# Kernel tuning notes

Measured on AMD Instinct MI355X. Metric: run time of the kernel, lower is better.

The kernel has to match this reference:

```python
import jax, jax.numpy as jnp
import numpy as np


def cheb_mats(N: int, degree: int):
    """Analysis/synthesis Chebyshev matrices, matching torch reference.
    Returns T_pinv [d+1, N], T_eval [N, d+1] as float32 jnp arrays."""
    x = np.linspace(0.0, 1.0, N, dtype=np.float32)
    xn = np.clip(2.0 * x - 1.0, -1 + 1e-06, 1 - 1e-06)
    theta = np.arccos(xn)
    ks = np.arange(degree + 1, dtype=np.float32)
    T = np.cos(theta[:, None] * ks[None, :])  # [N, d+1]
    T_pinv = np.linalg.pinv(T.astype(np.float64)).astype(np.float32)  # [d+1, N]
    return jnp.asarray(T_pinv), jnp.asarray(T.astype(np.float32))


def setup_inputs() -> dict:
    key = jax.random.key(0)
    k1, k2, k3 = jax.random.split(key, 3)
    B, C, H, W = 32, 64, 128, 128
    out_ch, degree = 64, 8
    scale_w = (2.0 / (C * (degree + 1))) ** 0.5
    scale_h = (2.0 / (out_ch * (degree + 1))) ** 0.5
    x = jax.random.normal(k1, (B, C, H, W), dtype=jnp.float32)
    W_w = scale_w * jax.random.normal(k2, (C, out_ch, degree + 1), dtype=jnp.float32)
    W_h = scale_h * jax.random.normal(k3, (out_ch, out_ch, degree + 1), dtype=jnp.float32)
    return {"x": x, "W_w": W_w, "W_h": W_h}


def reference(x, W_w, W_h):
    B, C, H, W = x.shape
    degree = W_w.shape[-1] - 1
    Tp_w, Te_w = cheb_mats(W, degree)  # [k,W], [W,k]
    Tp_h, Te_h = cheb_mats(H, degree)  # [k,H], [H,k]
    # --- mix along width axis with W_w (equivalent to torch's B*H batched 1D) ---
    c = jnp.einsum('bchw,kw->bchk', x, Tp_w)      # analysis: coeffs over width
    m = jnp.einsum('bchk,cok->bohk', c, W_w)      # channel mixing per degree
    y = jnp.einsum('bohk,wk->bohw', m, Te_w)      # synthesis back to width grid
    # --- mix along height axis with W_h ---
    c2 = jnp.einsum('bohw,kh->bokw', y, Tp_h)
    m2 = jnp.einsum('bokw,ofk->bfkw', c2, W_h)
    out = jnp.einsum('bfkw,hk->bfhw', m2, Te_h)   # [B, out_ch, H, W]
    return out
```

## Files before the change

### kernel.cpp

```cpp
#include <hip/hip_runtime.h>
#include <math.h>


#define K9 9

__global__ __launch_bounds__(256) void setup_all(const float* __restrict__ Ww,
                                                 const float* __restrict__ Wh,
                                                 float* __restrict__ Tp,
                                                 float* __restrict__ Te,
                                                 float* __restrict__ Tpt16,
                                                 float* __restrict__ Wt_w,
                                                 float* __restrict__ Wh_t) {
    int tid = threadIdx.x;
    if (blockIdx.x != 0) {
        int gid = (blockIdx.x - 1) * 256 + tid;
        if (gid < 36864) {
            int k = gid / 4096, r = gid % 4096, c = r / 64, o = r % 64;
            Wt_w[gid] = Ww[(c * 64 + o) * 9 + k];
        } else if (gid < 73728) {
            int g = gid - 36864;
            int k = g / 4096, r = g % 4096, o = r / 64, f = r % 64;
            Wh_t[g] = Wh[(o * 64 + f) * 9 + k];
        }
        return;
    }
    __shared__ double Tsh[128 * K9];
    __shared__ double GA[9][18];
    if (tid < 128) {
        int n = tid;
        float xf = (float)((double)n / 127.0);
        float xn = 2.0f * xf - 1.0f;
        const float lo = (float)(-1.0 + 1e-6);
        const float hi = (float)(1.0 - 1e-6);
        xn = fminf(fmaxf(xn, lo), hi);
        float th = acosf(xn);
        for (int k = 0; k < K9; ++k) {
            float tv = cosf(th * (float)k);
            Te[n * K9 + k] = tv;
            Tsh[n * K9 + k] = (double)tv;
        }
    }
    __syncthreads();
    if (tid < 81) {
        int i = tid / 9, j = tid % 9;
        double s = 0.0;
        for (int n = 0; n < 128; ++n) s += Tsh[n * K9 + i] * Tsh[n * K9 + j];
        GA[i][j] = s;
    }
    if (tid >= 81 && tid < 162) {
        int i = (tid - 81) / 9, j = (tid - 81) % 9;
        GA[i][9 + j] = (i == j) ? 1.0 : 0.0;
    }
    __syncthreads();
    int r18 = tid / 18, j18 = tid % 18;
    for (int col = 0; col < 9; ++col) {
        double inv = 0.0;
        if (tid < 18) inv = 1.0 / GA[col][col];
        __syncthreads();
        if (tid < 18) GA[col][tid] *= inv;
        __syncthreads();
        double f = 0.0;
        if (tid < 162 && r18 != col) f = GA[r18][col];
        __syncthreads();
        if (tid < 162 && r18 != col) GA[r18][j18] -= f * GA[col][j18];
        __syncthreads();
    }
    for (int idx = tid; idx < K9 * 128; idx += 256) {
        int k = idx / 128, n = idx % 128;
        double s = 0.0;
        for (int j = 0; j < 9; ++j) s += GA[k][9 + j] * Tsh[n * K9 + j];
        float sv = (float)s;
        Tp[idx] = sv;
        Tpt16[n * 16 + k] = sv;
    }
}

__global__ __launch_bounds__(256, 2) void k1_width(const float* __restrict__ x,
                                                   const float* __restrict__ Wt_w,
                                                   const float* __restrict__ Tpt16,
                                                   float* __restrict__ m_ws) {
    __shared__ float xs_red[2 * 64 * 129];
    __shared__ float cs[4 * 64 * K9];
    float* xs = xs_red;
    float* red = xs_red;
    int tid = threadIdx.x;
    int b  = blockIdx.x >> 5;
    int h0 = (blockIdx.x & 31) << 2;
    int c   = tid & 63;
    int wid = tid >> 6;
    int hh2 = wid >> 1;
    int q   = wid & 1;
    int qu  = __builtin_amdgcn_readfirstlane(q);
    const float* tpq = Tpt16 + qu * 64 * 16;
    const float* xb = x + (size_t)b * 1048576;

    for (int ch = 0; ch < 2; ++ch) {
        __syncthreads();
        for (int it = 0; it < 16; ++it) {
            int e = it * 256 + tid;
            int hh2s = e >> 11;
            int e2 = e & 2047;
            int cc = e2 >> 5;
            int w4 = (e2 & 31) << 2;
            float4 v = *(const float4*)(xb + (size_t)cc * 16384 +
                                        (size_t)(h0 + ch * 2 + hh2s) * 128 + w4);
            float* dst = &xs[hh2s * 8256 + cc * 129 + w4];
            dst[0] = v.x; dst[1] = v.y; dst[2] = v.z; dst[3] = v.w;
        }
        __syncthreads();
        float acc[K9];
#pragma unroll
        for (int k = 0; k < K9; ++k) acc[k] = 0.f;
        const float* xr = &xs[hh2 * 8256 + c * 129 + qu * 64];
#pragma unroll 8
        for (int w6 = 0; w6 < 64; ++w6) {
            float xv = xr[w6];
            const float* tr = tpq + w6 * 16;
#pragma unroll
            for (int k = 0; k < K9; ++k) acc[k] = fmaf(xv, tr[k], acc[k]);
        }
        __syncthreads();
        float* rw = &red[(wid * 64 + c) * K9];
#pragma unroll
        for (int k = 0; k < K9; ++k) rw[k] = acc[k];
        __syncthreads();
        for (int idx = tid; idx < 2 * 64 * K9; idx += 256) {
            int hh2r = idx / 576, rem = idx - hh2r * 576;
            float v0 = red[(2 * hh2r) * 576 + rem];
            float v1 = red[(2 * hh2r + 1) * 576 + rem];
            cs[(ch * 2 + hh2r) * 576 + rem] = v0 + v1;
        }
    }
    __syncthreads();
    float* mrow = m_ws + (size_t)(b * 128 + h0) * 576;
    for (int idx = tid; idx < 576; idx += 256) {
        int o = idx & 63, k = idx >> 6;
        const float* wt = Wt_w + k * 4096 + o;
        float a0 = 0.f, a1 = 0.f, a2 = 0.f, a3 = 0.f;
        for (int cc = 0; cc < 64; ++cc) {
            float wv = wt[cc * 64];
            float i0 = cs[0 * 576 + cc * 9 + k];
            float i1 = cs[1 * 576 + cc * 9 + k];
            float i2 = cs[2 * 576 + cc * 9 + k];
            float i3 = cs[3 * 576 + cc * 9 + k];
            a0 = fmaf(i0, wv, a0); a1 = fmaf(i1, wv, a1);
            a2 = fmaf(i2, wv, a2); a3 = fmaf(i3, wv, a3);
        }
        mrow[0 * 576 + idx] = a0;
        mrow[1 * 576 + idx] = a1;
        mrow[2 * 576 + idx] = a2;
        mrow[3 * 576 + idx] = a3;
    }
}

__global__ __launch_bounds__(256) void k2_height(const float* __restrict__ m_ws,
                                                 const float* __restrict__ Wh_t,
                                                 const float* __restrict__ Tp,
                                                 float* __restrict__ e_ws) {
    __shared__ float dl[576];
    int tid = threadIdx.x;
    int b  = blockIdx.x / K9;
    int kh = blockIdx.x - b * K9;
    const float* mb = m_ws + (size_t)b * 73728;
    const float* tpr = Tp + kh * 128;
    int p0 = tid, p1 = tid + 256, p2 = tid + 512;
    bool v2 = (p2 < 576);
    float a0 = 0.f, a1 = 0.f, a2 = 0.f;
#pragma unroll 4
    for (int h = 0; h < 128; ++h) {
        float tp = tpr[h];
        const float* mr = mb + (size_t)h * 576;
        a0 = fmaf(tp, mr[p0], a0);
        a1 = fmaf(tp, mr[p1], a1);
        if (v2) a2 = fmaf(tp, mr[p2], a2);
    }
    dl[p0] = a0;
    dl[p1] = a1;
    if (v2) dl[p2] = a2;
    __syncthreads();
    float* eb = e_ws + (size_t)b * 5184;
    for (int idx = tid; idx < 576; idx += 256) {
        int kw = idx >> 6, f = idx & 63;
        const float* wh = Wh_t + kh * 4096 + f;
        const float* dr = &dl[kw * 64];
        float acc = 0.f;
        for (int o = 0; o < 64; ++o)
            acc = fmaf(wh[o * 64], dr[o], acc);
        eb[(size_t)f * 81 + kh * 9 + kw] = acc;
    }
}

__global__ __launch_bounds__(256) void k3_synth(const float* __restrict__ e_ws,
                                                const float* __restrict__ Te,
                                                float* __restrict__ out) {
    __shared__ float tes[1152];
    __shared__ float el[81];
    __shared__ float f1[9 * 128];
    int tid = threadIdx.x;
    int bf = blockIdx.x;
    for (int i = tid; i < 1152; i += 256) tes[i] = Te[i];
    if (tid < 81) el[tid] = e_ws[(size_t)bf * 81 + tid];
    __syncthreads();
    for (int idx = tid; idx < 1152; idx += 256) {
        int kh = idx >> 7, w = idx & 127;
        float acc = 0.f;
#pragma unroll
        for (int kw = 0; kw < 9; ++kw)
            acc = fmaf(el[kh * 9 + kw], tes[w * 9 + kw], acc);
        f1[kh * 128 + w] = acc;
    }
    __syncthreads();
    int w4 = (tid & 31) << 2;
    int hg = tid >> 5;
    float4 fr[9];
#pragma unroll
    for (int k = 0; k < 9; ++k) fr[k] = *(const float4*)&f1[k * 128 + w4];
    float* ob = out + (size_t)bf * 16384;
    for (int h = hg; h < 128; h += 8) {
        const float* th = &tes[h * 9];
        float4 acc = make_float4(0.f, 0.f, 0.f, 0.f);
#pragma unroll
        for (int k = 0; k < 9; ++k) {
            float t = th[k];
            acc.x = fmaf(t, fr[k].x, acc.x);
            acc.y = fmaf(t, fr[k].y, acc.y);
            acc.z = fmaf(t, fr[k].z, acc.z);
            acc.w = fmaf(t, fr[k].w, acc.w);
        }
        *(float4*)(ob + h * 128 + w4) = acc;
    }
}

extern "C" void kernel_launch(void* const* d_in, const int* in_sizes, int n_in,
                              void* d_out, int out_size, void* d_ws, size_t ws_size,
                              hipStream_t stream) {
    (void)in_sizes; (void)n_in; (void)out_size; (void)ws_size;
    const float* x  = (const float*)d_in[0];
    const float* Ww = (const float*)d_in[1];
    const float* Wh = (const float*)d_in[2];
    float* out = (float*)d_out;
    float* ws = (float*)d_ws;
    float* Tp    = ws;
    float* Te    = ws + 1152;
    float* Tpt16 = ws + 2304;
    float* Wt_w  = ws + 4352;
    float* Wh_t  = ws + 41216;
    float* m_ws  = ws + 78080;
    float* e_ws  = ws + 78080 + 2359296;

    setup_all<<<289, 256, 0, stream>>>(Ww, Wh, Tp, Te, Tpt16, Wt_w, Wh_t);
    k1_width<<<1024, 256, 0, stream>>>(x, Wt_w, Tpt16, m_ws);
    k2_height<<<288, 256, 0, stream>>>(m_ws, Wh_t, Tp, e_ws);
    k3_synth<<<2048, 256, 0, stream>>>(e_ws, Te, out);
}
```

Baseline: 332.3 us.

## Fuse height analysis into width kernel via atomics and move height mixing into synthesis

The width kernel now projects its four-row channel-mixed coefficients onto the height Chebyshev basis and accumulates the result into a per-batch buffer with atomicAdd. This removes the large intermediate m_ws buffer and the separate k2_height kernel. The height channel mixing (W_h) is recomputed per (b,f) block inside the synthesis kernel from shared memory. The change drops one launch and the round trip of a ~9MB intermediate, at the cost of float atomic contention, nondeterministic summation order, a zeroing pass in setup, and redundant mixing work in each synthesis block.

New measurement: 299.7 us. 9.8% less time.

```diff
diff --git a/kernel.cpp b/kernel.cpp
--- a/kernel.cpp
+++ b/kernel.cpp
@@ -10,7 +10,8 @@
                                                  float* __restrict__ Te,
                                                  float* __restrict__ Tpt16,
                                                  float* __restrict__ Wt_w,
-                                                 float* __restrict__ Wh_t) {
+                                                 float* __restrict__ Wh_f,
+                                                 float* __restrict__ d_ws) {
     int tid = threadIdx.x;
     if (blockIdx.x != 0) {
         int gid = (blockIdx.x - 1) * 256 + tid;
@@ -19,8 +20,11 @@
             Wt_w[gid] = Ww[(c * 64 + o) * 9 + k];
         } else if (gid < 73728) {
             int g = gid - 36864;
-            int k = g / 4096, r = g % 4096, o = r / 64, f = r % 64;
-            Wh_t[g] = Wh[(o * 64 + f) * 9 + k];
+            int f = g / 576, r = g % 576, kh = r / 64, o = r % 64;
+            Wh_f[g] = Wh[(o * 64 + f) * 9 + kh];
+        } else if (gid < 115200) {
+            int g = gid - 73728;
+            ((float4*)d_ws)[g] = make_float4(0.f, 0.f, 0.f, 0.f);
         }
         return;
     }
@@ -78,7 +82,8 @@
 __global__ __launch_bounds__(256, 2) void k1_width(const float* __restrict__ x,
                                                    const float* __restrict__ Wt_w,
                                                    const float* __restrict__ Tpt16,
-                                                   float* __restrict__ m_ws) {
+                                                   const float* __restrict__ Tp,
+                                                   float* __restrict__ d_ws) {
     __shared__ float xs_red[2 * 64 * 129];
     __shared__ float cs[4 * 64 * K9];
     float* xs = xs_red;
@@ -132,7 +137,8 @@
         }
     }
     __syncthreads();
-    float* mrow = m_ws + (size_t)(b * 128 + h0) * 576;
+    float* db = d_ws + (size_t)b * 5184;
+    const float* tph = Tp + h0;
     for (int idx = tid; idx < 576; idx += 256) {
         int o = idx & 63, k = idx >> 6;
         const float* wt = Wt_w + k * 4096 + o;
@@ -146,60 +152,45 @@
             a0 = fmaf(i0, wv, a0); a1 = fmaf(i1, wv, a1);
             a2 = fmaf(i2, wv, a2); a3 = fmaf(i3, wv, a3);
         }
-        mrow[0 * 576 + idx] = a0;
-        mrow[1 * 576 + idx] = a1;
-        mrow[2 * 576 + idx] = a2;
-        mrow[3 * 576 + idx] = a3;
-    }
-}
-
-__global__ __launch_bounds__(256) void k2_height(const float* __restrict__ m_ws,
-                                                 const float* __restrict__ Wh_t,
-                                                 const float* __restrict__ Tp,
-                                                 float* __restrict__ e_ws) {
-    __shared__ float dl[576];
-    int tid = threadIdx.x;
-    int b  = blockIdx.x / K9;
-    int kh = blockIdx.x - b * K9;
-    const float* mb = m_ws + (size_t)b * 73728;
-    const float* tpr = Tp + kh * 128;
-    int p0 = tid, p1 = tid + 256, p2 = tid + 512;
-    bool v2 = (p2 < 576);
-    float a0 = 0.f, a1 = 0.f, a2 = 0.f;
-#pragma unroll 4
-    for (int h = 0; h < 128; ++h) {
-        float tp = tpr[h];
-        const float* mr = mb + (size_t)h * 576;
-        a0 = fmaf(tp, mr[p0], a0);
-        a1 = fmaf(tp, mr[p1], a1);
-        if (v2) a2 = fmaf(tp, mr[p2], a2);
-    }
-    dl[p0] = a0;
-    dl[p1] = a1;
-    if (v2) dl[p2] = a2;
-    __syncthreads();
-    float* eb = e_ws + (size_t)b * 5184;
-    for (int idx = tid; idx < 576; idx += 256) {
-        int kw = idx >> 6, f = idx & 63;
-        const float* wh = Wh_t + kh * 4096 + f;
-        const float* dr = &dl[kw * 64];
-        float acc = 0.f;
-        for (int o = 0; o < 64; ++o)
-            acc = fmaf(wh[o * 64], dr[o], acc);
-        eb[(size_t)f * 81 + kh * 9 + kw] = acc;
-    }
-}
-
-__global__ __launch_bounds__(256) void k3_synth(const float* __restrict__ e_ws,
+#pragma unroll
+        for (int kh = 0; kh < K9; ++kh) {
+            float t0 = tph[kh * 128 + 0];
+            float t1 = tph[kh * 128 + 1];
+            float t2 = tph[kh * 128 + 2];
+            float t3 = tph[kh * 128 + 3];
+            float contrib = fmaf(a0, t0, fmaf(a1, t1, fmaf(a2, t2, a3 * t3)));
+            atomicAdd(db + kh * 576 + idx, contrib);
+        }
+    }
+}
+
+__global__ __launch_bounds__(256) void k3_synth(const float* __restrict__ d_ws,
+                                                const float* __restrict__ Wh_f,
                                                 const float* __restrict__ Te,
                                                 float* __restrict__ out) {
+    __shared__ float ds[81 * 65];
+    __shared__ float whs[9 * 65];
     __shared__ float tes[1152];
+    __shared__ float f1[9 * 128];
     __shared__ float el[81];
-    __shared__ float f1[9 * 128];
     int tid = threadIdx.x;
     int bf = blockIdx.x;
+    int b = bf >> 6, f = bf & 63;
+    const float* db = d_ws + (size_t)b * 5184;
+    for (int i = tid; i < 5184; i += 256) ds[(i >> 6) * 65 + (i & 63)] = db[i];
+    const float* whf = Wh_f + (size_t)f * 576;
+    for (int i = tid; i < 576; i += 256) whs[(i >> 6) * 65 + (i & 63)] = whf[i];
     for (int i = tid; i < 1152; i += 256) tes[i] = Te[i];
-    if (tid < 81) el[tid] = e_ws[(size_t)bf * 81 + tid];
+    __syncthreads();
+    if (tid < 81) {
+        int kh = tid / 9;
+        const float* wr = &whs[kh * 65];
+        const float* dr = &ds[tid * 65];
+        float ea = 0.f;
+#pragma unroll 8
+        for (int o = 0; o < 64; ++o) ea = fmaf(wr[o], dr[o], ea);
+        el[tid] = ea;
+    }
     __syncthreads();
     for (int idx = tid; idx < 1152; idx += 256) {
         int kh = idx >> 7, w = idx & 127;
@@ -244,12 +235,10 @@
     float* Te    = ws + 1152;
     float* Tpt16 = ws + 2304;
     float* Wt_w  = ws + 4352;
-    float* Wh_t  = ws + 41216;
-    float* m_ws  = ws + 78080;
-    float* e_ws  = ws + 78080 + 2359296;
-
-    setup_all<<<289, 256, 0, stream>>>(Ww, Wh, Tp, Te, Tpt16, Wt_w, Wh_t);
-    k1_width<<<1024, 256, 0, stream>>>(x, Wt_w, Tpt16, m_ws);
-    k2_height<<<288, 256, 0, stream>>>(m_ws, Wh_t, Tp, e_ws);
-    k3_synth<<<2048, 256, 0, stream>>>(e_ws, Te, out);
-}
+    float* Wh_f  = ws + 41216;
+    float* d_d   = ws + 78080;
+
+    setup_all<<<451, 256, 0, stream>>>(Ww, Wh, Tp, Te, Tpt16, Wt_w, Wh_f, d_d);
+    k1_width<<<1024, 256, 0, stream>>>(x, Wt_w, Tpt16, Tp, d_d);
+    k3_synth<<<2048, 256, 0, stream>>>(d_d, Wh_f, Te, out);
+}
```
